# Optimization experiments

Measured on AMD Instinct MI355X. Metric: run time of the kernel, lower is better.

Reference implementation:

```python
import jax, jax.numpy as jnp
import numpy as np

EPS = 1e-5
B, N, M = 4, 256, 256
L, D, INNER = 6, 64, 64  # per-layer output = D//2 = 32 channels


def conv1x1(x, W, b=None):
    # x: [batch, Cin, H, W], W: [Cout, Cin]
    y = jnp.einsum('bchw,oc->bohw', x, W)
    if b is not None:
        y = y + b[None, :, None, None]
    return y


def batchnorm(x, g, b):
    # training-mode BN (default torch .train()): batch stats over (B, H, W)
    mu = x.mean(axis=(0, 2, 3), keepdims=True)
    var = x.var(axis=(0, 2, 3), keepdims=True)
    return g[None, :, None, None] * (x - mu) * jax.lax.rsqrt(var + EPS) + b[None, :, None, None]


def prelu(x, a):
    return jnp.where(x >= 0, x, a * x)


def cross_concat(Z):
    bs = Z.shape[0] // 2
    Za, Zb = Z[:bs], Z[bs:]
    return jnp.concatenate([jnp.concatenate([Za, Zb], 1),
                            jnp.concatenate([Zb, Za], 1)], 0)


def fw_layer(Z, Wm, bm, W, g, be, a):
    # FeatureWeavingLayer with EncoderMaxPool2stream
    bs = Z.shape[0] // 2
    X = cross_concat(Z)                                   # [2bs, 2C, N, M]
    z = conv1x1(X, Wm, bm)                                # [2bs, INNER, N, M]
    za = jnp.broadcast_to(z[:bs].max(axis=2, keepdims=True), z[:bs].shape)
    zb = jnp.broadcast_to(z[bs:].max(axis=3, keepdims=True), z[bs:].shape)
    z = jnp.concatenate([jnp.concatenate([X[:bs], za], 1),
                         jnp.concatenate([X[bs:], zb], 1)], 0)
    z = conv1x1(z, W)                                     # no bias
    z = batchnorm(z, g, be)
    return prelu(z, a)


def weavenet_fwd(Za, Zb, Wm0, bm0, W0, g0, be0, Wm, bm, W, g, be, a, Wf, gf, bf):
    Zb = jnp.swapaxes(Zb, -2, -1)      # [B, C, M, N] -> [B, C, N, M]
    Z = jnp.concatenate([Za, Zb], 0)   # [2B, 1, N, M]
    bs, n, m = Za.shape[0], Za.shape[-2], Za.shape[-1]
    layers = [(Wm0, bm0, W0, g0, be0)] + [(Wm[i], bm[i], W[i], g[i], be[i]) for i in range(L - 1)]
    Z_keep = None
    for i, (Wm_, bm_, W_, g_, be_) in enumerate(layers):
        Z = fw_layer(Z, Wm_, bm_, W_, g_, be_, a)
        if i % 2 == 0:  # use_resnet
            if Z_keep is not None:
                Z = Z + Z_keep
            Z_keep = Z
    Zc = conv1x1(cross_concat(Z), Wf)  # [2B, 1, N, M]
    Zc = batchnorm(Zc, gf, bf)
    m0 = Zc[:bs].reshape(bs, n, m)
    m1 = Zc[bs:].reshape(bs, n, m)
    # HV stream aggregation
    mm = (m0 + m1) / 2.0
    agg = jnp.minimum(jax.nn.softmax(mm, axis=-1), jax.nn.softmax(mm, axis=-2))
    return agg, m0, m1


def setup_inputs() -> dict:
    key = jax.random.key(0)
    ks = jax.random.split(key, 16)
    s = 0.05
    inp = {
        'Za': jax.random.normal(ks[0], (B, 1, N, M), jnp.float32),
        'Zb': jax.random.normal(ks[1], (B, 1, M, N), jnp.float32),
        # layer 0: input_dim = sab_dim*2 = 2
        'Wm0': jax.random.normal(ks[2], (INNER, 2), jnp.float32) * s,
        'bm0': jnp.zeros((INNER,), jnp.float32),
        'W0': jax.random.normal(ks[3], (D // 2, 2 + INNER), jnp.float32) * s,
        'g0': jnp.ones((D // 2,), jnp.float32),
        'be0': jnp.zeros((D // 2,), jnp.float32),
        # layers 1..L-1: input_dim = D = 64
        'Wm': jax.random.normal(ks[4], (L - 1, INNER, D), jnp.float32) * s,
        'bm': jnp.zeros((L - 1, INNER), jnp.float32),
        'W': jax.random.normal(ks[5], (L - 1, D // 2, D + INNER), jnp.float32) * s,
        'g': jnp.ones((L - 1, D // 2), jnp.float32),
        'be': jnp.zeros((L - 1, D // 2), jnp.float32),
        # shared PReLU (single default instance shared across all layers in torch)
        'a': jnp.float32(0.25),
        # final 1x1 conv (in = D after cross_concat) + BN
        'Wf': jax.random.normal(ks[6], (1, D), jnp.float32) * s,
        'gf': jnp.ones((1,), jnp.float32),
        'bf': jnp.zeros((1,), jnp.float32),
    }
    return inp


def reference(Za, Zb, Wm0, bm0, W0, g0, be0, Wm, bm, W, g, be, a, Wf, gf, bf):
    return weavenet_fwd(Za, Zb, Wm0, bm0, W0, g0, be0, Wm, bm, W, g, be, a, Wf, gf, bf)
```

## Files before the change

### kernel.cpp

```cpp
#include <hip/hip_runtime.h>

static constexpr int NMv  = 256;
static constexpr int PIXv = 65536;

__device__ __forceinline__ unsigned fkey(float f){
    unsigned b = __float_as_uint(f);
    return (b & 0x80000000u) ? ~b : (b | 0x80000000u);
}
__device__ __forceinline__ float unfkey(unsigned k){
    unsigned b = (k & 0x80000000u) ? (k & 0x7fffffffu) : ~k;
    return __uint_as_float(b);
}

__global__ __launch_bounds__(256) void k_prep(const float* __restrict__ Za,
                                              const float* __restrict__ Zb,
                                              float* __restrict__ Z){
    __shared__ float tile[32][33];
    int b  = blockIdx.z;
    int tx = threadIdx.x, ty = threadIdx.y;
    int n0 = blockIdx.y * 32, m0 = blockIdx.x * 32;
    if (b < 4){
        const float* src = Za + (size_t)b * PIXv;
        float*       dst = Z  + (size_t)b * PIXv;
        for (int j = 0; j < 32; j += 8){
            int n = n0 + ty + j;
            dst[n * NMv + m0 + tx] = src[n * NMv + m0 + tx];
        }
    } else {
        const float* src = Zb + (size_t)(b - 4) * PIXv;
        for (int j = 0; j < 32; j += 8)
            tile[ty + j][tx] = src[(m0 + ty + j) * NMv + n0 + tx];
        __syncthreads();
        float* dst = Z + (size_t)b * PIXv;
        for (int j = 0; j < 32; j += 8)
            dst[(n0 + ty + j) * NMv + m0 + tx] = tile[tx][ty + j];
    }
}

template<int C>
__global__ __launch_bounds__(256) void k_zmax(const float* __restrict__ Z,
                                              const float* __restrict__ Wm,
                                              const float* __restrict__ bm,
                                              unsigned* __restrict__ zkey){
    constexpr int K2 = 2 * C;
    __shared__ float Wms[K2 * 64];
    __shared__ float Xs[K2 * 68];
    int b = blockIdx.z;
    int t = threadIdx.x;
    for (int i = t; i < 64 * K2; i += 256){
        int c = i / K2, k = i % K2;
        Wms[k * 64 + c] = Wm[i];
    }
    const float* Z0 = Z + (size_t)b       * C * PIXv;
    const float* Z1 = Z + (size_t)(b ^ 4) * C * PIXv;

    if (b < 4){
        int m0 = blockIdx.x * 64, n0 = blockIdx.y * 16;
        int c0 = (t >> 3) * 2, mg = t & 7;
        float mx[2][8];
        #pragma unroll
        for (int a2 = 0; a2 < 2; a2++)
            #pragma unroll
            for (int j = 0; j < 8; j++) mx[a2][j] = -3.4e38f;
        for (int ni = 0; ni < 16; ni++){
            int n = n0 + ni;
            __syncthreads();
            for (int s = t; s < K2 * 16; s += 256){
                int k = s >> 4, m4 = (s & 15) * 4;
                const float* src = (k < C ? Z0 + (size_t)k * PIXv
                                          : Z1 + (size_t)(k - C) * PIXv) + n * NMv + m0 + m4;
                *(float4*)&Xs[k * 68 + m4] = *(const float4*)src;
            }
            __syncthreads();
            float acc[2][8];
            #pragma unroll
            for (int a2 = 0; a2 < 2; a2++)
                #pragma unroll
                for (int j = 0; j < 8; j++) acc[a2][j] = 0.f;
            #pragma unroll 8
            for (int k = 0; k < K2; k++){
                const float2 w  = *(const float2*)&Wms[k * 64 + c0];
                const float4 x0 = *(const float4*)&Xs[k * 68 + mg * 8];
                const float4 x1 = *(const float4*)&Xs[k * 68 + mg * 8 + 4];
                acc[0][0] += w.x * x0.x; acc[0][1] += w.x * x0.y;
                acc[0][2] += w.x * x0.z; acc[0][3] += w.x * x0.w;
                acc[0][4] += w.x * x1.x; acc[0][5] += w.x * x1.y;
                acc[0][6] += w.x * x1.z; acc[0][7] += w.x * x1.w;
                acc[1][0] += w.y * x0.x; acc[1][1] += w.y * x0.y;
                acc[1][2] += w.y * x0.z; acc[1][3] += w.y * x0.w;
                acc[1][4] += w.y * x1.x; acc[1][5] += w.y * x1.y;
                acc[1][6] += w.y * x1.z; acc[1][7] += w.y * x1.w;
            }
            #pragma unroll
            for (int a2 = 0; a2 < 2; a2++)
                #pragma unroll
                for (int j = 0; j < 8; j++) mx[a2][j] = fmaxf(mx[a2][j], acc[a2][j]);
        }
        #pragma unroll
        for (int a2 = 0; a2 < 2; a2++){
            float bmv = bm[c0 + a2];
            #pragma unroll
            for (int j = 0; j < 8; j++)
                atomicMax(&zkey[((size_t)b * 64 + c0 + a2) * NMv + m0 + mg * 8 + j],
                          fkey(mx[a2][j] + bmv));
        }
    } else {
        int n0 = blockIdx.x * 64, mq0 = blockIdx.y * 16;
        int c = t >> 2, mg = t & 3;
        float bmv = bm[c];
        for (int ni = 0; ni < 64; ni++){
            int n = n0 + ni;
            __syncthreads();
            for (int s = t; s < K2 * 4; s += 256){
                int k = s >> 2, m4 = (s & 3) * 4;
                const float* src = (k < C ? Z0 + (size_t)k * PIXv
                                          : Z1 + (size_t)(k - C) * PIXv) + n * NMv + mq0 + m4;
                *(float4*)&Xs[k * 20 + m4] = *(const float4*)src;
            }
            __syncthreads();
            float a0 = 0.f, a1 = 0.f, a2 = 0.f, a3 = 0.f;
            #pragma unroll 8
            for (int k = 0; k < K2; k++){
                const float  w = Wms[k * 64 + c];
                const float4 x = *(const float4*)&Xs[k * 20 + mg * 4];
                a0 += w * x.x; a1 += w * x.y; a2 += w * x.z; a3 += w * x.w;
            }
            float mx4 = fmaxf(fmaxf(a0, a1), fmaxf(a2, a3));
            mx4 = fmaxf(mx4, __shfl_xor(mx4, 1));
            mx4 = fmaxf(mx4, __shfl_xor(mx4, 2));
            if (mg == 0)
                atomicMax(&zkey[((size_t)b * 64 + c) * NMv + n], fkey(mx4 + bmv));
        }
    }
}

__global__ __launch_bounds__(256) void k_zmaxw(const unsigned* __restrict__ zkey,
                                               const float* __restrict__ W, int Wst,
                                               float* __restrict__ zmaxW){
    int oc = blockIdx.x, b = blockIdx.y, p = threadIdx.x;
    const float* wrow = W + (size_t)oc * Wst + (Wst - 64);
    float s = 0.f;
    #pragma unroll 8
    for (int c = 0; c < 64; c++)
        s += wrow[c] * unfkey(zkey[((size_t)b * 64 + c) * NMv + p]);
    zmaxW[((size_t)b * 32 + oc) * NMv + p] = s;
}

template<int C>
__global__ __launch_bounds__(256) void k_conv(const float* __restrict__ Z,
                                              const float* __restrict__ Wl,
                                              const float* __restrict__ zmaxW,
                                              float* __restrict__ Y,
                                              float* __restrict__ pstats){
    constexpr int K2 = 2 * C;
    constexpr int KC = (K2 < 16) ? K2 : 16;
    __shared__ float Ws[K2 * 32];
    __shared__ float Xs[KC * 256];
    int b   = blockIdx.y;
    int row = blockIdx.x;
    int t   = threadIdx.x;
    int p4  = t & 63, og = t >> 6;
    for (int i = t; i < K2 * 32; i += 256){
        int k = i >> 5, oc = i & 31;
        Ws[i] = Wl[(size_t)oc * (K2 + 64) + k];
    }
    const float* Z0 = Z + ((size_t)b       * C) * PIXv + (size_t)row * NMv;
    const float* Z1 = Z + ((size_t)(b ^ 4) * C) * PIXv + (size_t)row * NMv;
    float acc[4][8];
    #pragma unroll
    for (int j = 0; j < 4; j++)
        #pragma unroll
        for (int o = 0; o < 8; o++) acc[j][o] = 0.f;

    for (int kc = 0; kc < K2; kc += KC){
        __syncthreads();
        for (int s = t; s < KC * 64; s += 256){
            int k = kc + (s >> 6), m4 = (s & 63) * 4;
            const float* src = (k < C ? Z0 + (size_t)k * PIXv
                                      : Z1 + (size_t)(k - C) * PIXv) + m4;
            *(float4*)&Xs[(s >> 6) * 256 + m4] = *(const float4*)src;
        }
        __syncthreads();
        #pragma unroll 4
        for (int kk = 0; kk < KC; kk++){
            const float4 xv = *(const float4*)&Xs[kk * 256 + p4 * 4];
            const float4 wa = *(const float4*)&Ws[(kc + kk) * 32 + og * 8];
            const float4 wb = *(const float4*)&Ws[(kc + kk) * 32 + og * 8 + 4];
            const float xx[4] = {xv.x, xv.y, xv.z, xv.w};
            const float ww[8] = {wa.x, wa.y, wa.z, wa.w, wb.x, wb.y, wb.z, wb.w};
            #pragma unroll
            for (int j = 0; j < 4; j++)
                #pragma unroll
                for (int o = 0; o < 8; o++)
                    acc[j][o] += xx[j] * ww[o];
        }
    }
    if (b < 4){
        #pragma unroll
        for (int o = 0; o < 8; o++){
            float4 zw = *(const float4*)&zmaxW[((size_t)b * 32 + og * 8 + o) * NMv + p4 * 4];
            acc[0][o] += zw.x; acc[1][o] += zw.y; acc[2][o] += zw.z; acc[3][o] += zw.w;
        }
    } else {
        #pragma unroll
        for (int o = 0; o < 8; o++){
            float zw = zmaxW[((size_t)b * 32 + og * 8 + o) * NMv + row];
            acc[0][o] += zw; acc[1][o] += zw; acc[2][o] += zw; acc[3][o] += zw;
        }
    }
    float* yb = Y + ((size_t)b * 32 + og * 8) * PIXv + (size_t)row * NMv + p4 * 4;
    #pragma unroll
    for (int o = 0; o < 8; o++){
        float4 v = make_float4(acc[0][o], acc[1][o], acc[2][o], acc[3][o]);
        *(float4*)(yb + (size_t)o * PIXv) = v;
    }
    int blk = b * 256 + row;
    #pragma unroll
    for (int o = 0; o < 8; o++){
        float s1 = acc[0][o] + acc[1][o] + acc[2][o] + acc[3][o];
        float s2 = acc[0][o] * acc[0][o] + acc[1][o] * acc[1][o] +
                   acc[2][o] * acc[2][o] + acc[3][o] * acc[3][o];
        #pragma unroll
        for (int d = 32; d > 0; d >>= 1){
            s1 += __shfl_down(s1, d);
            s2 += __shfl_down(s2, d);
        }
        if ((t & 63) == 0){
            int c = og * 8 + o;
            pstats[(size_t)c        * 2048 + blk] = s1;
            pstats[(size_t)(32 + c) * 2048 + blk] = s2;
        }
    }
}

__global__ __launch_bounds__(256) void k_reduce(const float* __restrict__ src,
                                                float* __restrict__ dst){
    __shared__ float ls[4];
    int row = blockIdx.x, t = threadIdx.x;
    const float* p = src + (size_t)row * 2048 + t;
    float s = 0.f;
    #pragma unroll
    for (int j = 0; j < 8; j++) s += p[j * 256];
    #pragma unroll
    for (int d = 32; d > 0; d >>= 1) s += __shfl_down(s, d);
    if ((t & 63) == 0) ls[t >> 6] = s;
    __syncthreads();
    if (t == 0) dst[row] = ls[0] + ls[1] + ls[2] + ls[3];
}

__global__ __launch_bounds__(256) void k_bnapply(const float* __restrict__ Y,
                                                 const float* __restrict__ stats,
                                                 const float* __restrict__ g,
                                                 const float* __restrict__ be,
                                                 const float* __restrict__ keep_in,
                                                 const float* __restrict__ aptr,
                                                 float* __restrict__ Zout,
                                                 float* __restrict__ keep_out){
    __shared__ float s_sc[32], s_sh[32];
    if (threadIdx.x < 32){
        int c = threadIdx.x;
        const float inv = 1.f / (8.f * PIXv);
        float mu  = stats[c] * inv;
        float var = stats[32 + c] * inv - mu * mu;
        float sc  = g[c] * rsqrtf(var + 1e-5f);
        s_sc[c] = sc;
        s_sh[c] = be[c] - mu * sc;
    }
    __syncthreads();
    const float al = *aptr;
    const size_t tot = (size_t)8 * 32 * PIXv / 4;
    for (size_t i = (size_t)blockIdx.x * 256 + threadIdx.x; i < tot;
         i += (size_t)gridDim.x * 256){
        int c = (int)((i >> 14) & 31);
        float4 y = ((const float4*)Y)[i];
        float sc = s_sc[c], sh = s_sh[c];
        float4 v;
        v.x = sc * y.x + sh; v.y = sc * y.y + sh;
        v.z = sc * y.z + sh; v.w = sc * y.w + sh;
        v.x = v.x >= 0.f ? v.x : al * v.x;
        v.y = v.y >= 0.f ? v.y : al * v.y;
        v.z = v.z >= 0.f ? v.z : al * v.z;
        v.w = v.w >= 0.f ? v.w : al * v.w;
        if (keep_in){
            float4 kz = ((const float4*)keep_in)[i];
            v.x += kz.x; v.y += kz.y; v.z += kz.z; v.w += kz.w;
        }
        ((float4*)Zout)[i] = v;
        if (keep_out) ((float4*)keep_out)[i] = v;
    }
}

__global__ __launch_bounds__(256) void k_final(const float* __restrict__ Z,
                                               const float* __restrict__ Wf,
                                               float* __restrict__ T,
                                               float* __restrict__ pfin){
    int b = blockIdx.y;
    size_t base = (size_t)blockIdx.x * 1024 + (size_t)threadIdx.x * 4;
    const float* Z0 = Z + (size_t)b       * 32 * PIXv + base;
    const float* Z1 = Z + (size_t)(b ^ 4) * 32 * PIXv + base;
    float4 acc = make_float4(0.f, 0.f, 0.f, 0.f);
    #pragma unroll 8
    for (int c = 0; c < 32; c++){
        float w0 = Wf[c], w1 = Wf[32 + c];
        float4 x0 = *(const float4*)(Z0 + (size_t)c * PIXv);
        float4 x1 = *(const float4*)(Z1 + (size_t)c * PIXv);
        acc.x += w0 * x0.x + w1 * x1.x;
        acc.y += w0 * x0.y + w1 * x1.y;
        acc.z += w0 * x0.z + w1 * x1.z;
        acc.w += w0 * x0.w + w1 * x1.w;
    }
    *(float4*)(T + (size_t)b * PIXv + base) = acc;
    float a1 = acc.x + acc.y + acc.z + acc.w;
    float a2 = acc.x * acc.x + acc.y * acc.y + acc.z * acc.z + acc.w * acc.w;
    #pragma unroll
    for (int d = 32; d > 0; d >>= 1){
        a1 += __shfl_down(a1, d);
        a2 += __shfl_down(a2, d);
    }
    if ((threadIdx.x & 63) == 0){
        int slot = (blockIdx.y * 64 + blockIdx.x) * 4 + (threadIdx.x >> 6);
        pfin[slot]        = a1;
        pfin[2048 + slot] = a2;
    }
}

__global__ __launch_bounds__(256) void k_mm(const float* __restrict__ T,
                                            const float* __restrict__ fstats,
                                            const float* __restrict__ gf,
                                            const float* __restrict__ bf,
                                            float* __restrict__ out,
                                            float* __restrict__ MMb){
    const float inv = 1.f / (8.f * PIXv);
    float mu  = fstats[0] * inv;
    float var = fstats[1] * inv - mu * mu;
    float sc  = gf[0] * rsqrtf(var + 1e-5f);
    float sh  = bf[0] - mu * sc;
    size_t e = ((size_t)blockIdx.x * 256 + threadIdx.x) * 4;
    float4 t0 = *(const float4*)(T + e);
    float4 t1 = *(const float4*)(T + (size_t)4 * PIXv + e);
    float4 m0, m1, mv;
    m0.x = sc * t0.x + sh; m0.y = sc * t0.y + sh; m0.z = sc * t0.z + sh; m0.w = sc * t0.w + sh;
    m1.x = sc * t1.x + sh; m1.y = sc * t1.y + sh; m1.z = sc * t1.z + sh; m1.w = sc * t1.w + sh;
    mv.x = 0.5f * (m0.x + m1.x); mv.y = 0.5f * (m0.y + m1.y);
    mv.z = 0.5f * (m0.z + m1.z); mv.w = 0.5f * (m0.w + m1.w);
    *(float4*)(out + (size_t)4 * PIXv + e) = m0;
    *(float4*)(out + (size_t)8 * PIXv + e) = m1;
    *(float4*)(MMb + e) = mv;
}

__global__ __launch_bounds__(256) void k_rowstats(const float* __restrict__ MMb,
                                                  float* __restrict__ rmax,
                                                  float* __restrict__ rsum){
    int wid = threadIdx.x >> 6, lane = threadIdx.x & 63;
    int r = blockIdx.x * 4 + wid;
    const float* p = MMb + (size_t)r * NMv;
    float4 v = *(const float4*)(p + lane * 4);
    float mx = fmaxf(fmaxf(v.x, v.y), fmaxf(v.z, v.w));
    #pragma unroll
    for (int d = 32; d > 0; d >>= 1) mx = fmaxf(mx, __shfl_xor(mx, d));
    float s = expf(v.x - mx) + expf(v.y - mx) + expf(v.z - mx) + expf(v.w - mx);
    #pragma unroll
    for (int d = 32; d > 0; d >>= 1) s += __shfl_xor(s, d);
    if (lane == 0){ rmax[r] = mx; rsum[r] = s; }
}

__global__ __launch_bounds__(256) void k_colmax(const float* __restrict__ MMb,
                                                unsigned* __restrict__ ckey){
    int b = blockIdx.y, ch = blockIdx.x, m = threadIdx.x;
    const float* p = MMb + (size_t)b * PIXv + (size_t)ch * 16 * NMv + m;
    float mx = -3.4e38f;
    #pragma unroll
    for (int n = 0; n < 16; n++) mx = fmaxf(mx, p[(size_t)n * NMv]);
    atomicMax(&ckey[b * NMv + m], fkey(mx));
}
__global__ __launch_bounds__(256) void k_colsum(const float* __restrict__ MMb,
                                                const unsigned* __restrict__ ckey,
                                                float* __restrict__ csum){
    int b = blockIdx.y, ch = blockIdx.x, m = threadIdx.x;
    const float* p = MMb + (size_t)b * PIXv + (size_t)ch * 16 * NMv + m;
    float cm = unfkey(ckey[b * NMv + m]);
    float s = 0.f;
    #pragma unroll
    for (int n = 0; n < 16; n++) s += expf(p[(size_t)n * NMv] - cm);
    atomicAdd(&csum[b * NMv + m], s);
}

__global__ __launch_bounds__(256) void k_agg(const float* __restrict__ MMb,
                                             const float* __restrict__ rmax,
                                             const float* __restrict__ rsum,
                                             const unsigned* __restrict__ ckey,
                                             const float* __restrict__ csum,
                                             float* __restrict__ out){
    size_t e = ((size_t)blockIdx.x * 256 + threadIdx.x) * 4;
    int r = (int)(e >> 8);
    int b = (int)(e >> 16);
    int m = (int)(e & 255);
    int cb = b * NMv + m;
    float rm = rmax[r], rsi = 1.f / rsum[r];
    float4 v = *(const float4*)(MMb + e);
    float4 o;
    o.x = fminf(expf(v.x - rm) * rsi, expf(v.x - unfkey(ckey[cb + 0])) / csum[cb + 0]);
    o.y = fminf(expf(v.y - rm) * rsi, expf(v.y - unfkey(ckey[cb + 1])) / csum[cb + 1]);
    o.z = fminf(expf(v.z - rm) * rsi, expf(v.z - unfkey(ckey[cb + 2])) / csum[cb + 2]);
    o.w = fminf(expf(v.w - rm) * rsi, expf(v.w - unfkey(ckey[cb + 3])) / csum[cb + 3]);
    *(float4*)(out + e) = o;
}

extern "C" void kernel_launch(void* const* d_in, const int* in_sizes, int n_in,
                              void* d_out, int out_size, void* d_ws, size_t ws_size,
                              hipStream_t stream){
    (void)in_sizes; (void)n_in; (void)out_size; (void)ws_size;
    const float* Za  = (const float*)d_in[0];
    const float* Zb  = (const float*)d_in[1];
    const float* Wm0 = (const float*)d_in[2];
    const float* bm0 = (const float*)d_in[3];
    const float* W0  = (const float*)d_in[4];
    const float* g0  = (const float*)d_in[5];
    const float* be0 = (const float*)d_in[6];
    const float* Wm  = (const float*)d_in[7];
    const float* bm  = (const float*)d_in[8];
    const float* W   = (const float*)d_in[9];
    const float* g   = (const float*)d_in[10];
    const float* be  = (const float*)d_in[11];
    const float* ap  = (const float*)d_in[12];
    const float* Wf  = (const float*)d_in[13];
    const float* gf  = (const float*)d_in[14];
    const float* bf  = (const float*)d_in[15];
    float* out = (float*)d_out;

    size_t off = 0;
    char* wsb = (char*)d_ws;
    auto alloc = [&](size_t bytes) -> void* {
        void* p = wsb + off;
        off += (bytes + 255) & ~(size_t)255;
        return p;
    };
    float*    Zbuf  = (float*)   alloc((size_t)8 * 32 * PIXv * 4);
    float*    Zkeep = (float*)   alloc((size_t)8 * 32 * PIXv * 4);
    float*    Ybuf  = (float*)   alloc((size_t)8 * 32 * PIXv * 4);
    unsigned* zkey  = (unsigned*)alloc((size_t)8 * 64 * NMv * 4);
    float*    zmaxW = (float*)   alloc((size_t)8 * 32 * NMv * 4);
    float*    stats = (float*)   alloc(64 * 4);
    float*    T     = (float*)   alloc((size_t)8 * PIXv * 4);
    float*    fstats= (float*)   alloc(2 * 4);
    float*    MMb   = (float*)   alloc((size_t)4 * PIXv * 4);
    float*    rmaxb = (float*)   alloc(1024 * 4);
    float*    rsumb = (float*)   alloc(1024 * 4);
    unsigned* ckey  = (unsigned*)alloc(1024 * 4);
    float*    csum  = (float*)   alloc(1024 * 4);
    float*    pstats= (float*)   alloc((size_t)64 * 2048 * 4);
    float*    pfin  = (float*)   alloc((size_t)2 * 2048 * 4);

    k_prep<<<dim3(8, 8, 8), dim3(32, 8), 0, stream>>>(Za, Zb, Zbuf);

    for (int i = 0; i < 6; i++){
        const float *Wm_l, *bm_l, *W_l, *g_l, *be_l;
        int C;
        if (i == 0){ Wm_l = Wm0; bm_l = bm0; W_l = W0; g_l = g0; be_l = be0; C = 1; }
        else {
            Wm_l = Wm + (size_t)(i - 1) * 64 * 64;
            bm_l = bm + (size_t)(i - 1) * 64;
            W_l  = W  + (size_t)(i - 1) * 32 * 128;
            g_l  = g  + (size_t)(i - 1) * 32;
            be_l = be + (size_t)(i - 1) * 32;
            C = 32;
        }
        hipMemsetAsync(zkey, 0, (size_t)8 * 64 * NMv * 4, stream);
        if (C == 1) k_zmax<1 ><<<dim3(4, 16, 8), 256, 0, stream>>>(Zbuf, Wm_l, bm_l, zkey);
        else        k_zmax<32><<<dim3(4, 16, 8), 256, 0, stream>>>(Zbuf, Wm_l, bm_l, zkey);
        k_zmaxw<<<dim3(32, 8), 256, 0, stream>>>(zkey, W_l, 2 * C + 64, zmaxW);
        if (C == 1) k_conv<1 ><<<dim3(256, 8), 256, 0, stream>>>(Zbuf, W_l, zmaxW, Ybuf, pstats);
        else        k_conv<32><<<dim3(256, 8), 256, 0, stream>>>(Zbuf, W_l, zmaxW, Ybuf, pstats);
        k_reduce<<<64, 256, 0, stream>>>(pstats, stats);
        bool addk   = (i == 2 || i == 4);
        bool storek = (i % 2 == 0);
        k_bnapply<<<4096, 256, 0, stream>>>(Ybuf, stats, g_l, be_l,
                                            addk ? Zkeep : (const float*)nullptr, ap,
                                            Zbuf, storek ? Zkeep : (float*)nullptr);
    }

    k_final<<<dim3(64, 8), 256, 0, stream>>>(Zbuf, Wf, T, pfin);
    k_reduce<<<2, 256, 0, stream>>>(pfin, fstats);
    k_mm<<<256, 256, 0, stream>>>(T, fstats, gf, bf, out, MMb);
    k_rowstats<<<256, 256, 0, stream>>>(MMb, rmaxb, rsumb);
    hipMemsetAsync(ckey, 0, 1024 * 4, stream);
    hipMemsetAsync(csum, 0, 1024 * 4, stream);
    k_colmax<<<dim3(16, 4), 256, 0, stream>>>(MMb, ckey);
    k_colsum<<<dim3(16, 4), 256, 0, stream>>>(MMb, ckey, csum);
    k_agg<<<256, 256, 0, stream>>>(MMb, rmaxb, rsumb, ckey, csum, out);
}
```

Baseline: 1.393 ms.

## Unify zmax kernel paths, prefetch next row into registers, halve rows per block

The row-max branch of k_zmax now uses the same 64-column by 8-row tiling as the column-max branch, reducing across m with warp shuffles instead of the old narrow 16-column tiles that looped over 64 rows. Each row's global loads are issued into registers before the current row is computed, overlapping memory latency with the FMA loop. The block covers 8 rows instead of 16 and the grid doubles to compensate, adding parallelism. In exchange there are more atomicMax operations for the column-max results and more register pressure from the prefetch buffer.

```diff
diff --git a/kernel.cpp b/kernel.cpp
--- a/kernel.cpp
+++ b/kernel.cpp
@@ -42,7 +42,9 @@
                                               const float* __restrict__ Wm,
                                               const float* __restrict__ bm,
                                               unsigned* __restrict__ zkey){
-    constexpr int K2 = 2 * C;
+    constexpr int K2  = 2 * C;
+    constexpr int NCH = 8;
+    constexpr int NS  = (K2 * 16 + 255) / 256;
     __shared__ float Wms[K2 * 64];
     __shared__ float Xs[K2 * 68];
     int b = blockIdx.z;
@@ -53,83 +55,92 @@
     }
     const float* Z0 = Z + (size_t)b       * C * PIXv;
     const float* Z1 = Z + (size_t)(b ^ 4) * C * PIXv;
-
-    if (b < 4){
-        int m0 = blockIdx.x * 64, n0 = blockIdx.y * 16;
-        int c0 = (t >> 3) * 2, mg = t & 7;
-        float mx[2][8];
-        #pragma unroll
-        for (int a2 = 0; a2 < 2; a2++)
-            #pragma unroll
-            for (int j = 0; j < 8; j++) mx[a2][j] = -3.4e38f;
-        for (int ni = 0; ni < 16; ni++){
-            int n = n0 + ni;
-            __syncthreads();
-            for (int s = t; s < K2 * 16; s += 256){
+    int m0 = blockIdx.x * 64, n0 = blockIdx.y * NCH;
+    int c0 = (t >> 3) * 2, mg = t & 7;
+    float bmv0 = bm[c0], bmv1 = bm[c0 + 1];
+
+    float4 rbuf[NS];
+    auto issue = [&](int n){
+        #pragma unroll
+        for (int j = 0; j < NS; j++){
+            int s = t + j * 256;
+            if (s < K2 * 16){
                 int k = s >> 4, m4 = (s & 15) * 4;
                 const float* src = (k < C ? Z0 + (size_t)k * PIXv
                                           : Z1 + (size_t)(k - C) * PIXv) + n * NMv + m0 + m4;
-                *(float4*)&Xs[k * 68 + m4] = *(const float4*)src;
+                rbuf[j] = *(const float4*)src;
             }
-            __syncthreads();
-            float acc[2][8];
+        }
+    };
+    issue(n0);
+
+    float mx[2][8];
+    #pragma unroll
+    for (int a = 0; a < 2; a++)
+        #pragma unroll
+        for (int j = 0; j < 8; j++) mx[a][j] = -3.4e38f;
+
+    for (int ni = 0; ni < NCH; ni++){
+        __syncthreads();
+        #pragma unroll
+        for (int j = 0; j < NS; j++){
+            int s = t + j * 256;
+            if (s < K2 * 16){
+                int k = s >> 4, m4 = (s & 15) * 4;
+                *(float4*)&Xs[k * 68 + m4] = rbuf[j];
+            }
+        }
+        if (ni + 1 < NCH) issue(n0 + ni + 1);
+        __syncthreads();
+
+        float acc[2][8];
+        #pragma unroll
+        for (int a = 0; a < 2; a++)
             #pragma unroll
-            for (int a2 = 0; a2 < 2; a2++)
+            for (int j = 0; j < 8; j++) acc[a][j] = 0.f;
+        #pragma unroll 8
+        for (int k = 0; k < K2; k++){
+            const float2 w  = *(const float2*)&Wms[k * 64 + c0];
+            const float4 x0 = *(const float4*)&Xs[k * 68 + mg * 8];
+            const float4 x1 = *(const float4*)&Xs[k * 68 + mg * 8 + 4];
+            acc[0][0] += w.x * x0.x; acc[0][1] += w.x * x0.y;
+            acc[0][2] += w.x * x0.z; acc[0][3] += w.x * x0.w;
+            acc[0][4] += w.x * x1.x; acc[0][5] += w.x * x1.y;
+            acc[0][6] += w.x * x1.z; acc[0][7] += w.x * x1.w;
+            acc[1][0] += w.y * x0.x; acc[1][1] += w.y * x0.y;
+            acc[1][2] += w.y * x0.z; acc[1][3] += w.y * x0.w;
+            acc[1][4] += w.y * x1.x; acc[1][5] += w.y * x1.y;
+            acc[1][6] += w.y * x1.z; acc[1][7] += w.y * x1.w;
+        }
+
+        if (b < 4){
+            #pragma unroll
+            for (int a = 0; a < 2; a++)
                 #pragma unroll
-                for (int j = 0; j < 8; j++) acc[a2][j] = 0.f;
-            #pragma unroll 8
-            for (int k = 0; k < K2; k++){
-                const float2 w  = *(const float2*)&Wms[k * 64 + c0];
-                const float4 x0 = *(const float4*)&Xs[k * 68 + mg * 8];
-                const float4 x1 = *(const float4*)&Xs[k * 68 + mg * 8 + 4];
-                acc[0][0] += w.x * x0.x; acc[0][1] += w.x * x0.y;
-                acc[0][2] += w.x * x0.z; acc[0][3] += w.x * x0.w;
-                acc[0][4] += w.x * x1.x; acc[0][5] += w.x * x1.y;
-                acc[0][6] += w.x * x1.z; acc[0][7] += w.x * x1.w;
-                acc[1][0] += w.y * x0.x; acc[1][1] += w.y * x0.y;
-                acc[1][2] += w.y * x0.z; acc[1][3] += w.y * x0.w;
-                acc[1][4] += w.y * x1.x; acc[1][5] += w.y * x1.y;
-                acc[1][6] += w.y * x1.z; acc[1][7] += w.y * x1.w;
+                for (int j = 0; j < 8; j++) mx[a][j] = fmaxf(mx[a][j], acc[a][j]);
+        } else {
+            int n = n0 + ni;
+            #pragma unroll
+            for (int a = 0; a < 2; a++){
+                float v = fmaxf(fmaxf(fmaxf(acc[a][0], acc[a][1]), fmaxf(acc[a][2], acc[a][3])),
+                                fmaxf(fmaxf(acc[a][4], acc[a][5]), fmaxf(acc[a][6], acc[a][7])));
+                v = fmaxf(v, __shfl_xor(v, 1));
+                v = fmaxf(v, __shfl_xor(v, 2));
+                v = fmaxf(v, __shfl_xor(v, 4));
+                if (mg == 0)
+                    atomicMax(&zkey[((size_t)b * 64 + c0 + a) * NMv + n],
+                              fkey(v + (a ? bmv1 : bmv0)));
             }
-            #pragma unroll
-            for (int a2 = 0; a2 < 2; a2++)
-                #pragma unroll
-                for (int j = 0; j < 8; j++) mx[a2][j] = fmaxf(mx[a2][j], acc[a2][j]);
-        }
-        #pragma unroll
-        for (int a2 = 0; a2 < 2; a2++){
-            float bmv = bm[c0 + a2];
+        }
+    }
+    if (b < 4){
+        #pragma unroll
+        for (int a = 0; a < 2; a++){
+            float bmv = a ? bmv1 : bmv0;
             #pragma unroll
             for (int j = 0; j < 8; j++)
-                atomicMax(&zkey[((size_t)b * 64 + c0 + a2) * NMv + m0 + mg * 8 + j],
-                          fkey(mx[a2][j] + bmv));
-        }
-    } else {
-        int n0 = blockIdx.x * 64, mq0 = blockIdx.y * 16;
-        int c = t >> 2, mg = t & 3;
-        float bmv = bm[c];
-        for (int ni = 0; ni < 64; ni++){
-            int n = n0 + ni;
-            __syncthreads();
-            for (int s = t; s < K2 * 4; s += 256){
-                int k = s >> 2, m4 = (s & 3) * 4;
-                const float* src = (k < C ? Z0 + (size_t)k * PIXv
-                                          : Z1 + (size_t)(k - C) * PIXv) + n * NMv + mq0 + m4;
-                *(float4*)&Xs[k * 20 + m4] = *(const float4*)src;
-            }
-            __syncthreads();
-            float a0 = 0.f, a1 = 0.f, a2 = 0.f, a3 = 0.f;
-            #pragma unroll 8
-            for (int k = 0; k < K2; k++){
-                const float  w = Wms[k * 64 + c];
-                const float4 x = *(const float4*)&Xs[k * 20 + mg * 4];
-                a0 += w * x.x; a1 += w * x.y; a2 += w * x.z; a3 += w * x.w;
-            }
-            float mx4 = fmaxf(fmaxf(a0, a1), fmaxf(a2, a3));
-            mx4 = fmaxf(mx4, __shfl_xor(mx4, 1));
-            mx4 = fmaxf(mx4, __shfl_xor(mx4, 2));
-            if (mg == 0)
-                atomicMax(&zkey[((size_t)b * 64 + c) * NMv + n], fkey(mx4 + bmv));
+                atomicMax(&zkey[((size_t)b * 64 + c0 + a) * NMv + m0 + mg * 8 + j],
+                          fkey(mx[a][j] + bmv));
         }
     }
 }
@@ -466,8 +477,8 @@
             C = 32;
         }
         hipMemsetAsync(zkey, 0, (size_t)8 * 64 * NMv * 4, stream);
-        if (C == 1) k_zmax<1 ><<<dim3(4, 16, 8), 256, 0, stream>>>(Zbuf, Wm_l, bm_l, zkey);
-        else        k_zmax<32><<<dim3(4, 16, 8), 256, 0, stream>>>(Zbuf, Wm_l, bm_l, zkey);
+        if (C == 1) k_zmax<1 ><<<dim3(4, 32, 8), 256, 0, stream>>>(Zbuf, Wm_l, bm_l, zkey);
+        else        k_zmax<32><<<dim3(4, 32, 8), 256, 0, stream>>>(Zbuf, Wm_l, bm_l, zkey);
         k_zmaxw<<<dim3(32, 8), 256, 0, stream>>>(zkey, W_l, 2 * C + 64, zmaxW);
         if (C == 1) k_conv<1 ><<<dim3(256, 8), 256, 0, stream>>>(Zbuf, W_l, zmaxW, Ybuf, pstats);
         else        k_conv<32><<<dim3(256, 8), 256, 0, stream>>>(Zbuf, W_l, zmaxW, Ybuf, pstats);
```

Result: faster. 1.340 ms (-3.9%).
